# Kernel tuning notes

Measured on AMD Instinct MI355X. Metric: run time of the kernel, lower is better.

The kernel has to match this reference:

```python
import jax, jax.numpy as jnp
import numpy as np

N = 20000       # nodes
E = 160000      # edges (avg degree 8)
H = 8           # num_heads
D = 256         # model_dim
DV = D // H     # per-head value dim = 32
DR = 64         # deprel_edge_dim
DA = 64         # deparc_edge_dim
REL = DR + DA   # relation_dim = 128
RDV = REL // H  # per-head relation dim = 16
NB = 256        # neighbor_dim
N_DEPREL = 50
N_DEPARC = 4
EPS = 1e-12     # 1 / word.INFINITY_NUMBER
SLOPE = 0.2     # LeakyReLU slope


def _xavier(key, shape):
    fan_in, fan_out = shape[-2], shape[-1]
    lim = (6.0 / (fan_in + fan_out)) ** 0.5
    return jax.random.uniform(key, shape, jnp.float32, -lim, lim)


def setup_inputs() -> dict:
    ks = jax.random.split(jax.random.key(0), 16)
    return {
        'inp': jax.random.normal(ks[0], (N, D), jnp.float32),
        'dist_edge': jax.random.uniform(ks[1], (E,), jnp.float32) + 1.0,
        'W_value': _xavier(ks[2], (D, H * DV)),
        'W_relation': _xavier(ks[3], (REL, H * RDV)),
        'deprel_emb': jax.random.normal(ks[4], (N_DEPREL, DR), jnp.float32) * 0.02,
        'deparc_emb': jax.random.normal(ks[5], (N_DEPARC, DA), jnp.float32) * 0.02,
        'w_src': _xavier(ks[6], (H, DV)),
        'w_tgt': _xavier(ks[7], (H, DV)),
        'w_rel': _xavier(ks[8], (H, RDV)),
        'final_proj_w': _xavier(ks[9], (H, 2 * DV, DV)),
        'final_proj_b': jnp.zeros((H, DV), jnp.float32),
        'neighbor_w': _xavier(ks[10], (D, NB)),
        'neighbor_b': jnp.zeros((NB,), jnp.float32),
        'gate_w': _xavier(ks[11], (D + NB, H)),
        'gate_b': jnp.zeros((H,), jnp.float32),
        'final_bias': jnp.zeros((D,), jnp.float32),
        'edge_index': jax.random.randint(ks[12], (2, E), 0, N),
        'deprel_edge': jax.random.randint(ks[13], (E,), 1, N_DEPREL),
        'deparc_edge': jax.random.randint(ks[14], (E,), 1, N_DEPARC),
    }


def reference(inp, dist_edge, W_value, W_relation, deprel_emb, deparc_emb,
              w_src, w_tgt, w_rel, final_proj_w, final_proj_b,
              neighbor_w, neighbor_b, gate_w, gate_b, final_bias,
              edge_index, deprel_edge, deparc_edge):
    src, tgt = edge_index[0], edge_index[1]
    # value projection: [N, H, DV]
    value = (inp @ W_value).reshape(N, H, DV)
    # relation features from deprel/deparc embeddings: [E, REL] -> [E, H, RDV]
    rel_inp = jnp.concatenate([deprel_emb[deprel_edge], deparc_emb[deparc_edge]], axis=-1)
    relation = (rel_inp @ W_relation).reshape(E, H, RDV)
    # gather endpoints: [E, H, DV]
    node_src = value[src]
    node_tgt = value[tgt]
    leaky = lambda x: jnp.where(x >= 0, x, SLOPE * x)
    s_src = jnp.einsum('ehd,hd->eh', node_src, w_src)
    s_tgt = jnp.einsum('ehd,hd->eh', node_tgt, w_tgt)
    s_rel = jnp.einsum('ehr,hr->eh', relation, w_rel)
    scores_value = leaky(s_src + s_tgt)     # value-based attention scores [E, H]
    scores_relation = leaky(s_rel + s_tgt)  # relation-based attention scores [E, H]

    def aggregate(scores):
        # neighbor-aware softmax over incoming edges of each tgt node
        exp_s = jnp.exp(scores - scores.max())
        denom = jnp.zeros((N, H), exp_s.dtype).at[tgt].add(exp_s)[tgt]
        attn = exp_s / (denom + EPS)                       # [E, H]
        weighted = node_src * attn[:, :, None]             # [E, H, DV]
        return jnp.zeros((N, H, DV), weighted.dtype).at[tgt].add(weighted)

    out_v = aggregate(scores_value)      # [N, H, DV]
    out_r = aggregate(scores_relation)   # [N, H, DV]
    cat = jnp.concatenate([out_v, out_r], axis=-1)                   # [N, H, 2*DV]
    head_out = jnp.einsum('nhd,hdo->nho', cat, final_proj_w) + final_proj_b
    # gated head fusion: per-node per-head gate from input + mean neighbor feature
    nb = inp @ neighbor_w + neighbor_b                               # [N, NB]
    deg = jnp.zeros((N,), inp.dtype).at[tgt].add(1.0)
    nb_agg = jnp.zeros((N, NB), inp.dtype).at[tgt].add(nb[src]) / jnp.maximum(deg, 1.0)[:, None]
    gate = jax.nn.sigmoid(jnp.concatenate([inp, nb_agg], axis=-1) @ gate_w + gate_b)  # [N, H]
    return (head_out * gate[:, :, None]).reshape(N, D) + final_bias
```

## Files before the change

### kernel.cpp

```cpp
#include <hip/hip_runtime.h>
#include <hip/hip_fp16.h>
#include <math.h>

#define N_NODES 20000
#define N_EDGES 160000
#define EPSV 1e-12f
#define SLOPE 0.2f
#define LOG2E 1.4426950408889634f

__device__ __forceinline__ float leaky(float x) { return x >= 0.f ? x : SLOPE * x; }

__device__ __forceinline__ unsigned short cvt_bf16(float f) {
    unsigned u = __float_as_uint(f);
    u = (u + 0x7FFFu + ((u >> 16) & 1u)) >> 16;
    return (unsigned short)u;
}
__device__ __forceinline__ unsigned pk2(float a, float b) {
    return (unsigned)cvt_bf16(a) | ((unsigned)cvt_bf16(b) << 16);
}

__device__ __forceinline__ int btf_idx(int n, int k) {
    int w = n / 80, rem = n - w * 80, t = rem >> 4, l16 = rem & 15;
    int kk = k >> 5, c = k & 31, quad = c >> 3, e = c & 7;
    int lane = quad * 16 + l16;
    return (((w * 5 + t) * 8 + kk) * 64 + lane) * 8 + e;
}

typedef __attribute__((ext_vector_type(8))) short bf16x8;
typedef __attribute__((ext_vector_type(8))) _Float16 f16x8;
typedef __attribute__((ext_vector_type(4))) float f32x4;

__global__ __launch_bounds__(256) void k_pre(
    const float* __restrict__ Wv, const float* __restrict__ Wn,
    const float* __restrict__ nbb, const float* __restrict__ wsrc,
    const float* __restrict__ wtgt, const float* __restrict__ gw,
    unsigned short* __restrict__ Btf, float* __restrict__ bg2,
    const float* __restrict__ Wrel, const float* __restrict__ wrel,
    const float* __restrict__ deprel_emb, const float* __restrict__ deparc_emb,
    float* __restrict__ SA, float* __restrict__ SB,
    const int* __restrict__ tgt, int* __restrict__ cnts,
    const float* __restrict__ fpw, __half* __restrict__ Wpf,
    int* __restrict__ rss)
{
    __shared__ float wr2[128 * 8];
    __shared__ int cnt[250];
    __shared__ float gwc[256];
    __shared__ int wtot[4];
    int k = threadIdx.x;
    int b = blockIdx.x;
    if (b < 256) {
        Btf[btf_idx(b, k)] = cvt_bf16(Wv[k * 256 + b]);
    } else if (b < 264) {
        int h = b - 256;
        gwc[k] = gw[(256 + k) * 8 + h];
        __syncthreads();
        float a_vs = 0.f, a_vt = 0.f, a_ng = 0.f;
        for (int d = 0; d < 32; ++d) {
            float w = Wv[k * 256 + h * 32 + d];
            a_vs = fmaf(w, wsrc[h * 32 + d], a_vs);
            a_vt = fmaf(w, wtgt[h * 32 + d], a_vt);
        }
        const float4* wn4 = (const float4*)(Wn + (size_t)k * 256);
#pragma unroll 4
        for (int j = 0; j < 64; ++j) {
            float4 w4 = wn4[j];
            a_ng = fmaf(w4.x, gwc[j * 4 + 0], a_ng);
            a_ng = fmaf(w4.y, gwc[j * 4 + 1], a_ng);
            a_ng = fmaf(w4.z, gwc[j * 4 + 2], a_ng);
            a_ng = fmaf(w4.w, gwc[j * 4 + 3], a_ng);
        }
        Btf[btf_idx(256 + h, k)] = cvt_bf16(a_vs);
        Btf[btf_idx(264 + h, k)] = cvt_bf16(a_vt);
        Btf[btf_idx(272 + h, k)] = cvt_bf16(gw[k * 8 + h]);
        Btf[btf_idx(280 + h, k)] = cvt_bf16(a_ng);
        wr2[k] = nbb[k] * gwc[k];
        __syncthreads();
        if (k < 64) {
            float t = wr2[k] + wr2[k + 64] + wr2[k + 128] + wr2[k + 192];
#pragma unroll
            for (int off = 32; off; off >>= 1) t += __shfl_down(t, off, 64);
            if (k == 0) bg2[h] = t;
        }
    } else if (b < 272) {
        int n0 = 288 + (b - 264) * 4;
        for (int i = 0; i < 4; ++i) Btf[btf_idx(n0 + i, k)] = 0;
    } else if (b == 272) {
        for (int i = k; i < 1024; i += 256) {
            int kk = i >> 3, h = i & 7;
            float acc = 0.f;
            for (int r = 0; r < 16; ++r)
                acc += Wrel[kk * 128 + h * 16 + r] * wrel[h * 16 + r];
            wr2[kk * 8 + h] = acc;
        }
        __syncthreads();
        for (int i = k; i < 50 * 8; i += 256) {
            int d = i >> 3, h = i & 7;
            float acc = 0.f;
            for (int kk = 0; kk < 64; ++kk) acc += deprel_emb[d * 64 + kk] * wr2[kk * 8 + h];
            SA[i] = acc;
        }
        for (int i = k; i < 4 * 8; i += 256) {
            int d = i >> 3, h = i & 7;
            float acc = 0.f;
            for (int kk = 0; kk < 64; ++kk) acc += deparc_emb[d * 64 + kk] * wr2[(64 + kk) * 8 + h];
            SB[i] = acc;
        }
    } else if (b < 913) {
        int idx = b - 273;
        int slice = idx & 7, range = idx >> 3;
        int lo = range * 250;
        if (k < 250) cnt[k] = 0;
        __syncthreads();
        const int4* t4 = (const int4*)tgt;
        int i0 = slice * 5000;
        int mc = 0;
#pragma unroll 4
        for (int i = k; i < 5000; i += 256) {
            int4 v = t4[i0 + i];
            unsigned a = (unsigned)(v.x - lo); if (a < 250u) { atomicAdd(&cnt[a], 1); ++mc; }
            unsigned bb = (unsigned)(v.y - lo); if (bb < 250u) { atomicAdd(&cnt[bb], 1); ++mc; }
            unsigned c = (unsigned)(v.z - lo); if (c < 250u) { atomicAdd(&cnt[c], 1); ++mc; }
            unsigned d = (unsigned)(v.w - lo); if (d < 250u) { atomicAdd(&cnt[d], 1); ++mc; }
        }
        __syncthreads();
        if (k < 250) cnts[(lo + k) * 8 + slice] = cnt[k];
#pragma unroll
        for (int off = 32; off; off >>= 1) mc += __shfl_down(mc, off, 64);
        if ((k & 63) == 0) wtot[k >> 6] = mc;
        __syncthreads();
        if (k == 0) rss[idx] = wtot[0] + wtot[1] + wtot[2] + wtot[3];
    } else {
        for (int i = k; i < 2048; i += 256) {
            int lane = i & 63, kp = (i >> 6) & 1, jt = (i >> 7) & 1, h = i >> 8;
            int col = jt * 16 + (lane & 15);
            int krow = kp * 32 + (lane >> 4) * 8;
#pragma unroll
            for (int e = 0; e < 8; ++e)
                Wpf[(size_t)i * 8 + e] = __float2half(fpw[h * 2048 + (krow + e) * 32 + col]);
        }
    }
}

__global__ __launch_bounds__(256) void k_mid(
    const float* __restrict__ inp, const unsigned short* __restrict__ Btf,
    const float* __restrict__ bg2, __half* __restrict__ valh,
    float* __restrict__ vs, float* __restrict__ vt,
    float* __restrict__ g1, float* __restrict__ g2,
    const int* __restrict__ cnts, const int* __restrict__ rss,
    int* __restrict__ rowptr)
{
    __shared__ int red[4], red2[4];
    int tid = threadIdx.x;
    if (blockIdx.x < 1250) {
        int wave = tid >> 6, lane = tid & 63;
        int quad = lane >> 4, l16 = lane & 15;
        int row0 = blockIdx.x * 16;
        const float* arow = inp + (size_t)(row0 + l16) * 256;
        bf16x8 afr[8];
#pragma unroll
        for (int kk = 0; kk < 8; ++kk) {
            float4 f0 = *(const float4*)(arow + kk * 32 + quad * 8);
            float4 f1 = *(const float4*)(arow + kk * 32 + quad * 8 + 4);
            union { unsigned u[4]; bf16x8 v; } cv;
            cv.u[0] = pk2(f0.x, f0.y); cv.u[1] = pk2(f0.z, f0.w);
            cv.u[2] = pk2(f1.x, f1.y); cv.u[3] = pk2(f1.z, f1.w);
            afr[kk] = cv.v;
        }
        f32x4 acc[5] = {};
#pragma unroll
        for (int kk = 0; kk < 8; ++kk) {
#pragma unroll
            for (int t = 0; t < 5; ++t) {
                bf16x8 bf = *(const bf16x8*)(Btf + (((wave * 5 + t) * 8 + kk) * 64 + lane) * 8);
                acc[t] = __builtin_amdgcn_mfma_f32_16x16x32_bf16(afr[kk], bf, acc[t], 0, 0, 0);
            }
        }
#pragma unroll
        for (int t = 0; t < 5; ++t) {
            int n = wave * 80 + t * 16 + l16;
#pragma unroll
            for (int r = 0; r < 4; ++r) {
                int row = row0 + quad * 4 + r;
                float v = acc[t][r];
                if (n < 256) {
                    valh[(size_t)row * 256 + n] = __float2half(v);
                } else if (n < 288) {
                    int c2 = n - 256, which = c2 >> 3, h = c2 & 7;
                    if (which == 3) v += bg2[h];
                    float* dst = (which == 0) ? vs : (which == 1) ? vt : (which == 2) ? g1 : g2;
                    dst[(size_t)row * 8 + h] = v;
                }
            }
        }
    } else {
        int r = blockIdx.x - 1250;
        int lo = r * 250;
        int lane = tid & 63, w = tid >> 6;
        int m = r * 8;
        int part = 0;
        for (int i = tid; i < m; i += 256) part += rss[i];
#pragma unroll
        for (int off = 32; off; off >>= 1) part += __shfl_down(part, off, 64);
        if (lane == 0) red[w] = part;
        int deg = 0;
        if (tid < 250) {
            const int4* c4 = (const int4*)(cnts + (size_t)(lo + tid) * 8);
            int4 a = c4[0], b2 = c4[1];
            deg = a.x + a.y + a.z + a.w + b2.x + b2.y + b2.z + b2.w;
        }
        int ps = deg;
#pragma unroll
        for (int off = 1; off < 64; off <<= 1) {
            int x = __shfl_up(ps, off, 64);
            if (lane >= off) ps += x;
        }
        if (lane == 63) red2[w] = ps;
        __syncthreads();
        int base = red[0] + red[1] + red[2] + red[3];
        int wo = 0;
        for (int i = 0; i < w; ++i) wo += red2[i];
        if (tid < 250) rowptr[lo + tid] = base + wo + ps - deg;
        if (r == 79 && tid == 0) rowptr[N_NODES] = N_EDGES;
    }
}

__global__ __launch_bounds__(256) void k_fill(
    const int* __restrict__ src, const int* __restrict__ tgt,
    const int* __restrict__ deprel, const int* __restrict__ deparc,
    const int* __restrict__ rowptr, const int* __restrict__ cnts,
    int4* __restrict__ eidx4)
{
    __shared__ int cur[250];
    int tid = threadIdx.x;
    int slice = blockIdx.x & 7, range = blockIdx.x >> 3;
    int lo = range * 250;
    if (tid < 250) {
        int base = rowptr[lo + tid];
        const int* c = cnts + (size_t)(lo + tid) * 8;
        for (int s = 0; s < slice; ++s) base += c[s];
        cur[tid] = base;
    }
    __syncthreads();
    const int4* t4 = (const int4*)tgt;
    const int4* s4 = (const int4*)src;
    const int4* r4 = (const int4*)deprel;
    const int4* a4 = (const int4*)deparc;
    int i0 = slice * 5000;
    for (int i = tid; i < 5000; i += 256) {
        int4 v = t4[i0 + i];
        int4 sv = s4[i0 + i];
        int4 rv = r4[i0 + i];
        int4 av = a4[i0 + i];
        unsigned a = (unsigned)(v.x - lo); if (a < 250u) { int p = atomicAdd(&cur[a], 1); eidx4[p] = make_int4(sv.x, rv.x, av.x, 0); }
        unsigned b = (unsigned)(v.y - lo); if (b < 250u) { int p = atomicAdd(&cur[b], 1); eidx4[p] = make_int4(sv.y, rv.y, av.y, 0); }
        unsigned c = (unsigned)(v.z - lo); if (c < 250u) { int p = atomicAdd(&cur[c], 1); eidx4[p] = make_int4(sv.z, rv.z, av.z, 0); }
        unsigned d = (unsigned)(v.w - lo); if (d < 250u) { int p = atomicAdd(&cur[d], 1); eidx4[p] = make_int4(sv.w, rv.w, av.w, 0); }
    }
}

__global__ __launch_bounds__(256) void k_agg(
    const __half* __restrict__ valh, const float* __restrict__ vs,
    const float* __restrict__ vt, const float* __restrict__ SA,
    const float* __restrict__ SB, const float* __restrict__ g2,
    const float* __restrict__ g1, const float* __restrict__ gate_b,
    const int* __restrict__ rowptr, const int4* __restrict__ eidx4,
    const __half* __restrict__ Wpf, const float* __restrict__ Pb,
    const float* __restrict__ final_bias, float* __restrict__ out)
{
    __shared__ __half lds_cat[4][512];
    __shared__ float gate_lds[4][8];
    int tid = threadIdx.x, wv = tid >> 6, l = tid & 63;
    int n = blockIdx.x * 4 + wv;
    int beg = rowptr[n], end = rowptr[n + 1];
    int deg = end - beg;
    int h8 = l >> 3, q = l & 7;
    float vtq = vt[(size_t)n * 8 + q];

    float accV = 0.f, accR = 0.f, accG = 0.f;
    float4 av = make_float4(0, 0, 0, 0), ar = make_float4(0, 0, 0, 0);

    for (int base = beg; base < end; base += 64) {
        int cnt = min(64, end - base);
        int4 rec = make_int4(0, 0, 0, 0);
        if (l < cnt) rec = eidx4[base + l];
        for (int b0 = 0; b0 < cnt; b0 += 8) {
            int bn = min(8, cnt - b0);
            int se = __shfl(rec.x, b0 + h8, 64);
            int dr = __shfl(rec.y, b0 + h8, 64);
            int da = __shfl(rec.z, b0 + h8, 64);
            uint2 vvb[8];
#pragma unroll
            for (int p = 0; p < 8; ++p) {
                int pp = (p < bn) ? p : (bn - 1);
                int s1 = __shfl(se, pp << 3, 64);
                vvb[p] = *(const uint2*)(valh + (size_t)s1 * 256 + l * 4);
            }
            float eV = 0.f, eR = 0.f, gv = 0.f;
            if (h8 < bn) {
                float sa = vs[(size_t)se * 8 + q] + vtq;
                float sr = SA[dr * 8 + q] + SB[da * 8 + q] + vtq;
                eV = exp2f(leaky(sa) * LOG2E);
                eR = exp2f(leaky(sr) * LOG2E);
                gv = g2[(size_t)se * 8 + q];
            }
            accV += eV; accR += eR; accG += gv;
#pragma unroll
            for (int p = 0; p < 8; ++p) {
                if (p < bn) {
                    float wV = __shfl(eV, (p << 3) | h8, 64);
                    float wR = __shfl(eR, (p << 3) | h8, 64);
                    float2 f0 = __half22float2(*(__half2*)&vvb[p].x);
                    float2 f1 = __half22float2(*(__half2*)&vvb[p].y);
                    av.x = fmaf(f0.x, wV, av.x); av.y = fmaf(f0.y, wV, av.y);
                    av.z = fmaf(f1.x, wV, av.z); av.w = fmaf(f1.y, wV, av.w);
                    ar.x = fmaf(f0.x, wR, ar.x); ar.y = fmaf(f0.y, wR, ar.y);
                    ar.z = fmaf(f1.x, wR, ar.z); ar.w = fmaf(f1.y, wR, ar.w);
                }
            }
        }
    }
#pragma unroll
    for (int off = 8; off < 64; off <<= 1) {
        accV += __shfl_xor(accV, off, 64);
        accR += __shfl_xor(accR, off, 64);
        accG += __shfl_xor(accG, off, 64);
    }
    float rdv = 1.f / (__shfl(accV, h8, 64) + EPSV);
    float rdr = 1.f / (__shfl(accR, h8, 64) + EPSV);
    av.x *= rdv; av.y *= rdv; av.z *= rdv; av.w *= rdv;
    ar.x *= rdr; ar.y *= rdr; ar.z *= rdr; ar.w *= rdr;

    {
        __half* cp = &lds_cat[wv][h8 * 64 + q * 4];
        __half2 a01 = __floats2half2_rn(av.x, av.y);
        __half2 a23 = __floats2half2_rn(av.z, av.w);
        __half2 r01 = __floats2half2_rn(ar.x, ar.y);
        __half2 r23 = __floats2half2_rn(ar.z, ar.w);
        uint2 sa_; sa_.x = *(unsigned*)&a01; sa_.y = *(unsigned*)&a23;
        uint2 sr_; sr_.x = *(unsigned*)&r01; sr_.y = *(unsigned*)&r23;
        *(uint2*)cp = sa_;
        *(uint2*)(cp + 32) = sr_;
    }
    if (l < 8) {
        float dscale = 1.f / (float)(deg > 1 ? deg : 1);
        float gl = g1[(size_t)n * 8 + l] + accG * dscale + gate_b[l];
        gate_lds[wv][l] = 1.f / (1.f + exp2f(-gl * LOG2E));
    }
    __syncthreads();

    int n0 = blockIdx.x * 4;
    int l16 = l & 15, hi = l >> 4;
#pragma unroll
    for (int hp = 0; hp < 2; ++hp) {
        int h = wv * 2 + hp;
        f32x4 acc0 = {0.f, 0.f, 0.f, 0.f}, acc1 = {0.f, 0.f, 0.f, 0.f};
#pragma unroll
        for (int kp = 0; kp < 2; ++kp) {
            f16x8 afr = {};
            if (l16 < 4) afr = *(const f16x8*)(&lds_cat[l16][h * 64 + kp * 32 + hi * 8]);
            f16x8 bf0 = *(const f16x8*)(Wpf + (size_t)(((h * 2 + 0) * 2 + kp) * 64 + l) * 8);
            f16x8 bf1 = *(const f16x8*)(Wpf + (size_t)(((h * 2 + 1) * 2 + kp) * 64 + l) * 8);
            acc0 = __builtin_amdgcn_mfma_f32_16x16x32_f16(afr, bf0, acc0, 0, 0, 0);
            acc1 = __builtin_amdgcn_mfma_f32_16x16x32_f16(afr, bf1, acc1, 0, 0, 0);
        }
        if (hi == 0) {
            float pb0 = Pb[h * 32 + l16],        pb1 = Pb[h * 32 + 16 + l16];
            float fb0 = final_bias[h * 32 + l16], fb1 = final_bias[h * 32 + 16 + l16];
#pragma unroll
            for (int r = 0; r < 4; ++r) {
                int row = n0 + r;
                float g = gate_lds[r][h];
                out[(size_t)row * 256 + h * 32 + l16]      = fmaf(acc0[r] + pb0, g, fb0);
                out[(size_t)row * 256 + h * 32 + 16 + l16] = fmaf(acc1[r] + pb1, g, fb1);
            }
        }
    }
}

extern "C" void kernel_launch(void* const* d_in, const int* in_sizes, int n_in,
                              void* d_out, int out_size, void* d_ws, size_t ws_size,
                              hipStream_t stream) {
    const float* inp         = (const float*)d_in[0];
    const float* W_value     = (const float*)d_in[2];
    const float* W_relation  = (const float*)d_in[3];
    const float* deprel_emb  = (const float*)d_in[4];
    const float* deparc_emb  = (const float*)d_in[5];
    const float* w_src       = (const float*)d_in[6];
    const float* w_tgt       = (const float*)d_in[7];
    const float* w_rel       = (const float*)d_in[8];
    const float* fpw         = (const float*)d_in[9];
    const float* fpb         = (const float*)d_in[10];
    const float* neighbor_w  = (const float*)d_in[11];
    const float* neighbor_b  = (const float*)d_in[12];
    const float* gate_w      = (const float*)d_in[13];
    const float* gate_b      = (const float*)d_in[14];
    const float* final_bias  = (const float*)d_in[15];
    const int*   edge_index  = (const int*)d_in[16];
    const int*   deprel_edge = (const int*)d_in[17];
    const int*   deparc_edge = (const int*)d_in[18];
    const int* srcArr = edge_index;
    const int* tgtArr = edge_index + N_EDGES;
    float* out = (float*)d_out;

    __half* valh = (__half*)d_ws;
    unsigned short* Btf = (unsigned short*)(valh + 5120000);
    float* bg2 = (float*)(Btf + 81920);
    float* vs = bg2 + 8;
    float* vt = vs + 160000;
    float* g1 = vt + 160000;
    float* g2 = g1 + 160000;
    float* SA = g2 + 160000;
    float* SB = SA + 400;
    int* cnts = (int*)(SB + 32);
    int* rowptr = cnts + 160000;
    int4* eidx4 = (int4*)(rowptr + 20004);
    __half* Wpf = (__half*)(eidx4 + 160000);
    int* rss = (int*)(Wpf + 16384);

    k_pre<<<914, 256, 0, stream>>>(W_value, neighbor_w, neighbor_b,
                                   w_src, w_tgt, gate_w, Btf, bg2,
                                   W_relation, w_rel, deprel_emb, deparc_emb, SA, SB,
                                   tgtArr, cnts, fpw, Wpf, rss);
    k_mid<<<1330, 256, 0, stream>>>(inp, Btf, bg2, valh, vs, vt, g1, g2, cnts, rss, rowptr);
    k_fill<<<640, 256, 0, stream>>>(srcArr, tgtArr, deprel_edge, deparc_edge,
                                    rowptr, cnts, eidx4);
    k_agg<<<N_NODES / 4, 256, 0, stream>>>(valh, vs, vt, SA, SB, g2, g1, gate_b,
                                           rowptr, eidx4, Wpf, fpb, final_bias, out);
}
```

Measured before the change: 179.8 us.

## Precompute per-edge score and gate records in CSR fill kernel

```diff
diff --git a/kernel.cpp b/kernel.cpp
--- a/kernel.cpp
+++ b/kernel.cpp
@@ -224,11 +224,37 @@
     }
 }
 
+__device__ __forceinline__ void fill_rec(
+    int p, int s, int dr, int da,
+    int* __restrict__ eidx, float* __restrict__ esc,
+    const float* __restrict__ vs, const float* __restrict__ SA,
+    const float* __restrict__ SB, const float* __restrict__ g2)
+{
+    eidx[p] = s;
+    float* ep = esc + (size_t)p * 24;
+    const float4* vp = (const float4*)(vs + (size_t)s * 8);
+    const float4* ap = (const float4*)(SA + dr * 8);
+    const float4* bp = (const float4*)(SB + da * 8);
+    const float4* gp = (const float4*)(g2 + (size_t)s * 8);
+    float4 v0 = vp[0], v1 = vp[1];
+    float4 a0 = ap[0], a1 = ap[1];
+    float4 b0 = bp[0], b1 = bp[1];
+    float4 g0 = gp[0], g1v = gp[1];
+    ((float4*)ep)[0] = v0;
+    ((float4*)ep)[1] = v1;
+    ((float4*)ep)[2] = make_float4(a0.x + b0.x, a0.y + b0.y, a0.z + b0.z, a0.w + b0.w);
+    ((float4*)ep)[3] = make_float4(a1.x + b1.x, a1.y + b1.y, a1.z + b1.z, a1.w + b1.w);
+    ((float4*)ep)[4] = g0;
+    ((float4*)ep)[5] = g1v;
+}
+
 __global__ __launch_bounds__(256) void k_fill(
     const int* __restrict__ src, const int* __restrict__ tgt,
     const int* __restrict__ deprel, const int* __restrict__ deparc,
     const int* __restrict__ rowptr, const int* __restrict__ cnts,
-    int4* __restrict__ eidx4)
+    const float* __restrict__ vs, const float* __restrict__ SA,
+    const float* __restrict__ SB, const float* __restrict__ g2,
+    int* __restrict__ eidx, float* __restrict__ esc)
 {
     __shared__ int cur[250];
     int tid = threadIdx.x;
@@ -251,19 +277,18 @@
         int4 sv = s4[i0 + i];
         int4 rv = r4[i0 + i];
         int4 av = a4[i0 + i];
-        unsigned a = (unsigned)(v.x - lo); if (a < 250u) { int p = atomicAdd(&cur[a], 1); eidx4[p] = make_int4(sv.x, rv.x, av.x, 0); }
-        unsigned b = (unsigned)(v.y - lo); if (b < 250u) { int p = atomicAdd(&cur[b], 1); eidx4[p] = make_int4(sv.y, rv.y, av.y, 0); }
-        unsigned c = (unsigned)(v.z - lo); if (c < 250u) { int p = atomicAdd(&cur[c], 1); eidx4[p] = make_int4(sv.z, rv.z, av.z, 0); }
-        unsigned d = (unsigned)(v.w - lo); if (d < 250u) { int p = atomicAdd(&cur[d], 1); eidx4[p] = make_int4(sv.w, rv.w, av.w, 0); }
+        unsigned a = (unsigned)(v.x - lo); if (a < 250u) { int p = atomicAdd(&cur[a], 1); fill_rec(p, sv.x, rv.x, av.x, eidx, esc, vs, SA, SB, g2); }
+        unsigned b = (unsigned)(v.y - lo); if (b < 250u) { int p = atomicAdd(&cur[b], 1); fill_rec(p, sv.y, rv.y, av.y, eidx, esc, vs, SA, SB, g2); }
+        unsigned c = (unsigned)(v.z - lo); if (c < 250u) { int p = atomicAdd(&cur[c], 1); fill_rec(p, sv.z, rv.z, av.z, eidx, esc, vs, SA, SB, g2); }
+        unsigned d = (unsigned)(v.w - lo); if (d < 250u) { int p = atomicAdd(&cur[d], 1); fill_rec(p, sv.w, rv.w, av.w, eidx, esc, vs, SA, SB, g2); }
     }
 }
 
 __global__ __launch_bounds__(256) void k_agg(
-    const __half* __restrict__ valh, const float* __restrict__ vs,
-    const float* __restrict__ vt, const float* __restrict__ SA,
-    const float* __restrict__ SB, const float* __restrict__ g2,
+    const __half* __restrict__ valh, const float* __restrict__ vt,
     const float* __restrict__ g1, const float* __restrict__ gate_b,
-    const int* __restrict__ rowptr, const int4* __restrict__ eidx4,
+    const int* __restrict__ rowptr, const int* __restrict__ eidx,
+    const float* __restrict__ esc,
     const __half* __restrict__ Wpf, const float* __restrict__ Pb,
     const float* __restrict__ final_bias, float* __restrict__ out)
 {
@@ -281,13 +306,16 @@
 
     for (int base = beg; base < end; base += 64) {
         int cnt = min(64, end - base);
-        int4 rec = make_int4(0, 0, 0, 0);
-        if (l < cnt) rec = eidx4[base + l];
+        int rec = 0;
+        if (l < cnt) rec = eidx[base + l];
         for (int b0 = 0; b0 < cnt; b0 += 8) {
             int bn = min(8, cnt - b0);
-            int se = __shfl(rec.x, b0 + h8, 64);
-            int dr = __shfl(rec.y, b0 + h8, 64);
-            int da = __shfl(rec.z, b0 + h8, 64);
+            int se = __shfl(rec, b0 + h8, 64);
+            int ei = base + b0 + ((h8 < bn) ? h8 : (bn - 1));
+            const float* ep = esc + (size_t)ei * 24;
+            float sVv = ep[q];
+            float sRv = ep[8 + q];
+            float gvv = ep[16 + q];
             uint2 vvb[8];
 #pragma unroll
             for (int p = 0; p < 8; ++p) {
@@ -297,11 +325,9 @@
             }
             float eV = 0.f, eR = 0.f, gv = 0.f;
             if (h8 < bn) {
-                float sa = vs[(size_t)se * 8 + q] + vtq;
-                float sr = SA[dr * 8 + q] + SB[da * 8 + q] + vtq;
-                eV = exp2f(leaky(sa) * LOG2E);
-                eR = exp2f(leaky(sr) * LOG2E);
-                gv = g2[(size_t)se * 8 + q];
+                eV = exp2f(leaky(sVv + vtq) * LOG2E);
+                eR = exp2f(leaky(sRv + vtq) * LOG2E);
+                gv = gvv;
             }
             accV += eV; accR += eR; accG += gv;
 #pragma unroll
@@ -413,9 +439,10 @@
     float* SB = SA + 400;
     int* cnts = (int*)(SB + 32);
     int* rowptr = cnts + 160000;
-    int4* eidx4 = (int4*)(rowptr + 20004);
-    __half* Wpf = (__half*)(eidx4 + 160000);
+    int* eidx = rowptr + 20004;
+    __half* Wpf = (__half*)(eidx + 160000);
     int* rss = (int*)(Wpf + 16384);
+    float* esc = (float*)(rss + 640);
 
     k_pre<<<914, 256, 0, stream>>>(W_value, neighbor_w, neighbor_b,
                                    w_src, w_tgt, gate_w, Btf, bg2,
@@ -423,7 +450,7 @@
                                    tgtArr, cnts, fpw, Wpf, rss);
     k_mid<<<1330, 256, 0, stream>>>(inp, Btf, bg2, valh, vs, vt, g1, g2, cnts, rss, rowptr);
     k_fill<<<640, 256, 0, stream>>>(srcArr, tgtArr, deprel_edge, deparc_edge,
-                                    rowptr, cnts, eidx4);
-    k_agg<<<N_NODES / 4, 256, 0, stream>>>(valh, vs, vt, SA, SB, g2, g1, gate_b,
-                                           rowptr, eidx4, Wpf, fpb, final_bias, out);
-}
+                                    rowptr, cnts, vs, SA, SB, g2, eidx, esc);
+    k_agg<<<N_NODES / 4, 256, 0, stream>>>(valh, vt, g1, gate_b,
+                                           rowptr, eidx, esc, Wpf, fpb, final_bias, out);
+}
```

Result: slower. 232.8 us (+29.5%).
